# Kernel optimization log

Measured on AMD Instinct MI355X. Metric: run time of the kernel, lower is better.

## Reference

```python
import jax, jax.numpy as jnp
import numpy as np

B, W, H, V, L = 64, 512, 1024, 32000, 2


def setup_inputs() -> dict:
    key = jax.random.key(0)
    ks = jax.random.split(key, 20)
    s = 0.02  # init scale
    n = lambda k, shp: jax.random.normal(k, shp, jnp.float32)
    return {
        "input": jax.random.randint(ks[0], (B, 1), 0, V),
        "h0": n(ks[1], (L, B, H)),
        "c0": n(ks[2], (L, B, H)),
        "encoder_output": n(ks[3], (B, W, H)),
        "embedding": n(ks[4], (V, H)) * s,
        "W_ih0": n(ks[5], (4 * H, H)) * s,
        "W_hh0": n(ks[6], (4 * H, H)) * s,
        "b_ih0": n(ks[7], (4 * H,)) * s,
        "b_hh0": n(ks[8], (4 * H,)) * s,
        "W_ih1": n(ks[9], (4 * H, H)) * s,
        "W_hh1": n(ks[10], (4 * H, H)) * s,
        "b_ih1": n(ks[11], (4 * H,)) * s,
        "b_hh1": n(ks[12], (4 * H,)) * s,
        "att_w": n(ks[13], (2 * H,)) * s,
        "att_b": n(ks[14], (1,)) * s,
        "input_W": n(ks[15], (H, 2 * H)) * s,
        "input_b": n(ks[16], (H,)) * s,
        "out_W": n(ks[17], (V, H)) * s,
        "out_b": n(ks[18], (V,)) * s,
    }


def _lstm_step(x, h, c, W_ih, W_hh, b_ih, b_hh):
    # PyTorch gate order: i, f, g, o
    g = x @ W_ih.T + h @ W_hh.T + b_ih + b_hh
    i, f, gg, o = jnp.split(g, 4, axis=-1)
    c2 = jax.nn.sigmoid(f) * c + jax.nn.sigmoid(i) * jnp.tanh(gg)
    return jax.nn.sigmoid(o) * jnp.tanh(c2), c2


def reference(input, h0, c0, encoder_output, embedding,
              W_ih0, W_hh0, b_ih0, b_hh0, W_ih1, W_hh1, b_ih1, b_hh1,
              att_w, att_b, input_W, input_b, out_W, out_b):
    Hd = h0.shape[-1]
    emb = embedding[input]                       # (B,1,H)
    att_state = h0[-1] * c0[-1]                  # (B,H)
    # Vectorized replacement of the per-word cat+linear loop:
    # att_line(cat(enc_w, att_state)) = enc_w @ w_enc + att_state @ w_st + b
    w_enc, w_st = att_w[:Hd], att_w[Hd:]
    scores = encoder_output @ w_enc + (att_state @ w_st)[:, None] + att_b[0]  # (B,W)
    # Original quirk: weigth starts with a zeros column, then softmax over
    # weigth[:, 0:-1] -> zero column + scores for words 0..W-2 (last dropped).
    zeros = jnp.zeros((scores.shape[0], 1), scores.dtype)
    full = jnp.concatenate([zeros, scores[:, :-1]], axis=1)  # (B,W)
    wts = jax.nn.softmax(full, axis=1)
    ctx = jnp.einsum('bw,bwh->bh', wts, encoder_output)      # (B,H)
    x = jnp.concatenate([ctx, emb[:, 0, :]], axis=-1)        # (B,2H)
    x = x @ input_W.T + input_b                              # (B,H)
    h1, c1 = _lstm_step(x, h0[0], c0[0], W_ih0, W_hh0, b_ih0, b_hh0)
    h2, c2 = _lstm_step(h1, h0[1], c0[1], W_ih1, W_hh1, b_ih1, b_hh1)
    logits = h2 @ out_W.T + out_b                            # (B,V)
    logp = jax.nn.log_softmax(logits, axis=-1)[:, None, :]   # (B,1,V)
    return logp, jnp.stack([h1, h2]), jnp.stack([c1, c2])
```

## Files before the change

### kernel.cpp

```cpp
#include <hip/hip_runtime.h>
#include <hip/hip_bf16.h>

#define Bsz 64
#define Wln 512
#define Hd  1024
#define Vc  32000

typedef short v8s __attribute__((ext_vector_type(8)));
typedef float f32x4 __attribute__((ext_vector_type(4)));

__device__ inline unsigned short f2b(float f) {
  union { float f; unsigned u; } v; v.f = f;
  return (unsigned short)((v.u + 0x8000u) >> 16);
}
__device__ inline float wave_sum(float v) {
  #pragma unroll
  for (int o = 32; o; o >>= 1) v += __shfl_down(v, o);
  return v;
}
__device__ inline float wave_max(float v) {
  #pragma unroll
  for (int o = 32; o; o >>= 1) v = fmaxf(v, __shfl_down(v, o));
  return v;
}
__device__ inline float sigm(float x) { return 1.f / (1.f + expf(-x)); }

__device__ inline v8s cvt_frag(float4 x0, float4 x1) {
  v8s r;
  r[0] = (short)f2b(x0.x); r[1] = (short)f2b(x0.y);
  r[2] = (short)f2b(x0.z); r[3] = (short)f2b(x0.w);
  r[4] = (short)f2b(x1.x); r[5] = (short)f2b(x1.y);
  r[6] = (short)f2b(x1.z); r[7] = (short)f2b(x1.w);
  return r;
}

__global__ __launch_bounds__(256) void k_satt_emb(
    const float* __restrict__ h0, const float* __restrict__ c0,
    const float* __restrict__ att_w, const float* __restrict__ att_b,
    const int* __restrict__ input, const float* __restrict__ emb,
    float* __restrict__ s_att, float* __restrict__ cat)
{
  int b = blockIdx.x, t = threadIdx.x;
  int idx = input[b];
  for (int j = t; j < Hd; j += 256)
    cat[b * 2 * Hd + Hd + j] = emb[(size_t)idx * Hd + j];
  size_t base = (size_t)(Bsz + b) * Hd;
  float s = 0.f;
  for (int j = t; j < Hd; j += 256)
    s += h0[base + j] * c0[base + j] * att_w[Hd + j];
  s = wave_sum(s);
  __shared__ float red[4];
  if ((t & 63) == 0) red[t >> 6] = s;
  __syncthreads();
  if (t == 0) s_att[b] = red[0] + red[1] + red[2] + red[3] + att_b[0];
}

__global__ __launch_bounds__(256) void k_scores(
    const float* __restrict__ enc, const float* __restrict__ att_w,
    const float* __restrict__ s_att, float* __restrict__ scores)
{
  int row = blockIdx.x * 4 + (threadIdx.x >> 6);
  int lane = threadIdx.x & 63;
  const float* p = enc + (size_t)row * Hd + lane * 16;
  const float* w = att_w + lane * 16;
  float s = 0.f;
  #pragma unroll
  for (int c = 0; c < 4; ++c) {
    float4 e = *(const float4*)(p + c * 4);
    float4 ww = *(const float4*)(w + c * 4);
    s += e.x * ww.x + e.y * ww.y + e.z * ww.z + e.w * ww.w;
  }
  s = wave_sum(s);
  if (lane == 0) scores[row] = s + s_att[row >> 9];
}

__global__ __launch_bounds__(512) void k_softmax(
    const float* __restrict__ scores, float* __restrict__ wts)
{
  int b = blockIdx.x, t = threadIdx.x;
  float v = (t == 0) ? 0.f : scores[b * Wln + t - 1];
  __shared__ float redm[8], reds[8];
  float m = wave_max(v);
  if ((t & 63) == 0) redm[t >> 6] = m;
  __syncthreads();
  m = redm[0];
  #pragma unroll
  for (int i = 1; i < 8; ++i) m = fmaxf(m, redm[i]);
  float e = expf(v - m);
  float s = wave_sum(e);
  if ((t & 63) == 0) reds[t >> 6] = s;
  __syncthreads();
  s = reds[0];
  #pragma unroll
  for (int i = 1; i < 8; ++i) s += reds[i];
  wts[b * Wln + t] = e / s;
}

__global__ __launch_bounds__(256) void k_ctx_part(
    const float* __restrict__ wts, const float* __restrict__ enc,
    float* __restrict__ part)
{
  int b = blockIdx.x >> 3, ch = blockIdx.x & 7;
  int t = threadIdx.x;
  __shared__ float w[64];
  if (t < 64) w[t] = wts[b * Wln + ch * 64 + t];
  __syncthreads();
  int h4 = t * 4;
  const float* p = enc + (size_t)b * Wln * Hd + (size_t)ch * 64 * Hd + h4;
  float a0 = 0, a1 = 0, a2 = 0, a3 = 0;
  #pragma unroll 4
  for (int i = 0; i < 64; ++i) {
    float4 e = *(const float4*)(p + (size_t)i * Hd);
    float wi = w[i];
    a0 += wi * e.x; a1 += wi * e.y; a2 += wi * e.z; a3 += wi * e.w;
  }
  float* o = part + ((size_t)b * 8 + ch) * Hd + h4;
  o[0] = a0; o[1] = a1; o[2] = a2; o[3] = a3;
}

__global__ __launch_bounds__(256) void k_ctx_red(
    const float* __restrict__ part, float* __restrict__ cat)
{
  int idx = blockIdx.x * 256 + threadIdx.x;
  int b = idx >> 10, h = idx & 1023;
  float s = 0.f;
  #pragma unroll
  for (int c = 0; c < 8; ++c) s += part[((size_t)b * 8 + c) * Hd + h];
  cat[b * 2 * Hd + h] = s;
}

template<int NS>
__global__ __launch_bounds__(512) void gemm_v4(
    const float* __restrict__ A1, const float* __restrict__ A1b, int sA1,
    const float* __restrict__ B1, int sB1, const float* __restrict__ bias1,
    float* __restrict__ out1,
    const float* __restrict__ A2, const float* __restrict__ A2b, int sA2,
    const float* __restrict__ B2, int sB2, const float* __restrict__ bias2,
    float* __restrict__ out2,
    int N, int nblk1)
{
  constexpr int KS  = 8 / NS;
  constexpr int KSL = 1024 / KS;
  const int tid = threadIdx.x;

  const float *A, *Ab, *B, *bias; float* out; int sA, sB, bid;
  if ((int)blockIdx.x < nblk1) {
    A = A1; Ab = A1b; sA = sA1; B = B1; sB = sB1; bias = bias1; out = out1;
    bid = blockIdx.x;
  } else {
    A = A2; Ab = A2b; sA = sA2; B = B2; sB = sB2; bias = bias2; out = out2;
    bid = blockIdx.x - nblk1;
  }

  __shared__ __align__(16) char pool[131072];

  #pragma unroll
  for (int it = 0; it < 16; ++it) {
    int idx = it * 512 + tid;
    int row = idx >> 7, ch = idx & 127;
    const float* src = A + (size_t)row * sA + ch * 8;
    float4 x0 = *(const float4*)src;
    float4 x1 = *(const float4*)(src + 4);
    if (Ab) {
      const float* s2 = Ab + (size_t)row * sA + ch * 8;
      float4 y0 = *(const float4*)s2;
      float4 y1 = *(const float4*)(s2 + 4);
      x0.x += y0.x; x0.y += y0.y; x0.z += y0.z; x0.w += y0.w;
      x1.x += y1.x; x1.y += y1.y; x1.z += y1.z; x1.w += y1.w;
    }
    *(v8s*)(pool + row * 2048 + ((ch * 16) ^ ((row & 7) << 4))) = cvt_frag(x0, x1);
  }
  __syncthreads();

  const int w = tid >> 6, lane = tid & 63;
  const int r = lane & 15, q = lane >> 4;
  const int nsub = w % NS, kh = w / NS;
  const int n0 = bid * (NS * 16);

  f32x4 acc[4] = {{0,0,0,0},{0,0,0,0},{0,0,0,0},{0,0,0,0}};
  const float* bp = B + (size_t)(n0 + nsub * 16 + r) * sB + kh * KSL + q * 8;
  const int swz = (r & 7) << 4;

  #pragma unroll 4
  for (int kk = 0; kk < KSL / 32; ++kk) {
    float4 b0 = *(const float4*)(bp + kk * 32);
    float4 b1 = *(const float4*)(bp + kk * 32 + 4);
    v8s bf = cvt_frag(b0, b1);
    int cb = ((kh * KSL + kk * 32 + q * 8) * 2) ^ swz;
    #pragma unroll
    for (int m = 0; m < 4; ++m) {
      v8s af = *(const v8s*)(pool + (m * 16 + r) * 2048 + cb);
      acc[m] = __builtin_amdgcn_mfma_f32_16x16x32_bf16(af, bf, acc[m], 0, 0, 0);
    }
  }

  __syncthreads();
  float (*red)[64][17] = (float(*)[64][17])pool;
  #pragma unroll
  for (int m = 0; m < 4; ++m)
    #pragma unroll
    for (int rr = 0; rr < 4; ++rr)
      red[w][lane][m * 4 + rr] = acc[m][rr];
  __syncthreads();

  constexpr int COLS = NS * 16;
  #pragma unroll
  for (int it = 0; it < NS * 2; ++it) {
    int e = it * 512 + tid;
    int cc = e % COLS, rowi = e / COLS;
    int ns2 = cc >> 4, lo = cc & 15;
    int idx = ((rowi >> 4) << 2) + (rowi & 3);
    int le  = (((rowi >> 2) & 3) << 4) + lo;
    float s = 0.f;
    #pragma unroll
    for (int j = 0; j < KS; ++j) s += red[ns2 + j * NS][le][idx];
    float bb = bias ? bias[n0 + cc] : 0.f;
    out[(size_t)rowi * N + n0 + cc] = s + bb;
  }
}

__global__ __launch_bounds__(256) void k_lstm(
    const float* __restrict__ g1, const float* __restrict__ g2,
    const float* __restrict__ c0,
    float* __restrict__ out_h, float* __restrict__ out_c)
{
  int b = blockIdx.x >> 2;
  int j = ((blockIdx.x & 3) << 8) + threadIdx.x;
  const float* ga = g1 + (size_t)b * 4 * Hd;
  const float* gb = g2 + (size_t)b * 4 * Hd;
  float gi = ga[j] + gb[j];
  float gf = ga[Hd + j] + gb[Hd + j];
  float gg = ga[2 * Hd + j] + gb[2 * Hd + j];
  float go = ga[3 * Hd + j] + gb[3 * Hd + j];
  float c = sigm(gf) * c0[(size_t)b * Hd + j] + sigm(gi) * tanhf(gg);
  float h = sigm(go) * tanhf(c);
  out_h[b * Hd + j] = h;
  out_c[b * Hd + j] = c;
}

__global__ __launch_bounds__(1024) void k_logsoftmax(float* __restrict__ lg)
{
  int b = blockIdx.x, t = threadIdx.x;
  float* row = lg + (size_t)b * Vc;
  __shared__ float red[16];
  float m = -1e30f;
  for (int w = t; w < Vc; w += 1024) m = fmaxf(m, row[w]);
  m = wave_max(m);
  if ((t & 63) == 0) red[t >> 6] = m;
  __syncthreads();
  float M = red[0];
  #pragma unroll
  for (int i = 1; i < 16; ++i) M = fmaxf(M, red[i]);
  __syncthreads();
  float s = 0.f;
  for (int w = t; w < Vc; w += 1024) s += expf(row[w] - M);
  s = wave_sum(s);
  if ((t & 63) == 0) red[t >> 6] = s;
  __syncthreads();
  float S = red[0];
  #pragma unroll
  for (int i = 1; i < 16; ++i) S += red[i];
  float lse = M + logf(S);
  for (int w = t; w < Vc; w += 1024) row[w] = row[w] - lse;
}

extern "C" void kernel_launch(void* const* d_in, const int* in_sizes, int n_in,
                              void* d_out, int out_size, void* d_ws, size_t ws_size,
                              hipStream_t stream)
{
  const int*   input = (const int*)d_in[0];
  const float* h0    = (const float*)d_in[1];
  const float* c0    = (const float*)d_in[2];
  const float* enc   = (const float*)d_in[3];
  const float* emb   = (const float*)d_in[4];
  const float* W_ih0 = (const float*)d_in[5];
  const float* W_hh0 = (const float*)d_in[6];
  const float* b_ih0 = (const float*)d_in[7];
  const float* b_hh0 = (const float*)d_in[8];
  const float* W_ih1 = (const float*)d_in[9];
  const float* W_hh1 = (const float*)d_in[10];
  const float* b_ih1 = (const float*)d_in[11];
  const float* b_hh1 = (const float*)d_in[12];
  const float* att_w = (const float*)d_in[13];
  const float* att_b = (const float*)d_in[14];
  const float* inW   = (const float*)d_in[15];
  const float* inb   = (const float*)d_in[16];
  const float* outW  = (const float*)d_in[17];
  const float* outb  = (const float*)d_in[18];
  float* out = (float*)d_out;

  char* sc = (char*)d_out;
  float* g1     = (float*)(sc + 0);
  float* g2     = (float*)(sc + 1048576);
  float* ctxp   = (float*)(sc + 2097152);
  float* cat    = (float*)(sc + 4194304);
  float* x1     = (float*)(sc + 4718592);
  float* x2     = (float*)(sc + 4980736);
  float* scores = (float*)(sc + 5242880);
  float* s_att  = (float*)(sc + 5373952);

  float* out_h = out + (size_t)Bsz * Vc;
  float* out_c = out_h + 2 * Bsz * Hd;
  float* h1 = out_h;
  float* h2 = out_h + Bsz * Hd;

  k_satt_emb<<<Bsz, 256, 0, stream>>>(h0, c0, att_w, att_b, input, emb, s_att, cat);
  k_scores<<<Bsz * Wln / 4, 256, 0, stream>>>(enc, att_w, s_att, scores);
  k_softmax<<<Bsz, 512, 0, stream>>>(scores, scores);
  k_ctx_part<<<Bsz * 8, 256, 0, stream>>>(scores, enc, ctxp);
  k_ctx_red<<<Bsz * Hd / 256, 256, 0, stream>>>(ctxp, cat);

  gemm_v4<1><<<128, 512, 0, stream>>>(
      cat,        nullptr, 2 * Hd, inW,      2 * Hd, inb,     x1,
      cat + Hd,   nullptr, 2 * Hd, inW + Hd, 2 * Hd, nullptr, x2,
      Hd, 64);

  gemm_v4<2><<<256, 512, 0, stream>>>(
      x1, x2,      Hd, W_ih0, Hd, b_ih0, g1,
      h0, nullptr, Hd, W_hh0, Hd, b_hh0, g2,
      4 * Hd, 128);
  k_lstm<<<Bsz * 4, 256, 0, stream>>>(g1, g2, c0, h1, out_c);

  gemm_v4<2><<<256, 512, 0, stream>>>(
      h1,                     nullptr, Hd, W_ih1, Hd, b_ih1, g1,
      h0 + (size_t)Bsz * Hd,  nullptr, Hd, W_hh1, Hd, b_hh1, g2,
      4 * Hd, 128);
  k_lstm<<<Bsz * 4, 256, 0, stream>>>(g1, g2, c0 + (size_t)Bsz * Hd, h2, out_c + Bsz * Hd);

  gemm_v4<4><<<500, 512, 0, stream>>>(
      h2,      nullptr, Hd, outW,    Hd, outb,    out,
      nullptr, nullptr, 0,  nullptr, 0,  nullptr, nullptr,
      Vc, 500);
  k_logsoftmax<<<Bsz, 1024, 0, stream>>>(out);
}
```

Before: 149.8 us.

## Fuse attention kernels and fold context reduction into input GEMM load

Merges the score and state-attention kernels into one launch and folds the softmax into the context-partial kernel, which recomputes the max and sum per chunk block. Adds a mode to the GEMM A-load that sums the 8 context partials, removing the separate reduction kernel and the concat buffer. Log-softmax switches to a single-pass online max/sum, and the GEMM k-loop is fully unrolled. Fewer launches and less global traffic come at the cost of redundant softmax work in every ctx block and heavier GEMM prologue loads.

New measurement: 174.1 us. 16.2% more time.

```diff
diff --git a/kernel.cpp b/kernel.cpp
--- a/kernel.cpp
+++ b/kernel.cpp
@@ -34,122 +34,109 @@
   return r;
 }
 
-__global__ __launch_bounds__(256) void k_satt_emb(
+__global__ __launch_bounds__(256) void k_scores_satt(
+    const float* __restrict__ enc, const float* __restrict__ att_w,
     const float* __restrict__ h0, const float* __restrict__ c0,
-    const float* __restrict__ att_w, const float* __restrict__ att_b,
-    const int* __restrict__ input, const float* __restrict__ emb,
-    float* __restrict__ s_att, float* __restrict__ cat)
-{
-  int b = blockIdx.x, t = threadIdx.x;
-  int idx = input[b];
-  for (int j = t; j < Hd; j += 256)
-    cat[b * 2 * Hd + Hd + j] = emb[(size_t)idx * Hd + j];
-  size_t base = (size_t)(Bsz + b) * Hd;
-  float s = 0.f;
-  for (int j = t; j < Hd; j += 256)
-    s += h0[base + j] * c0[base + j] * att_w[Hd + j];
-  s = wave_sum(s);
+    const float* __restrict__ att_b, const int* __restrict__ input,
+    const float* __restrict__ emb,
+    float* __restrict__ scores, float* __restrict__ s_att,
+    float* __restrict__ embbuf)
+{
   __shared__ float red[4];
-  if ((t & 63) == 0) red[t >> 6] = s;
-  __syncthreads();
-  if (t == 0) s_att[b] = red[0] + red[1] + red[2] + red[3] + att_b[0];
-}
-
-__global__ __launch_bounds__(256) void k_scores(
-    const float* __restrict__ enc, const float* __restrict__ att_w,
-    const float* __restrict__ s_att, float* __restrict__ scores)
-{
-  int row = blockIdx.x * 4 + (threadIdx.x >> 6);
-  int lane = threadIdx.x & 63;
-  const float* p = enc + (size_t)row * Hd + lane * 16;
-  const float* w = att_w + lane * 16;
-  float s = 0.f;
-  #pragma unroll
-  for (int c = 0; c < 4; ++c) {
-    float4 e = *(const float4*)(p + c * 4);
-    float4 ww = *(const float4*)(w + c * 4);
-    s += e.x * ww.x + e.y * ww.y + e.z * ww.z + e.w * ww.w;
-  }
-  s = wave_sum(s);
-  if (lane == 0) scores[row] = s + s_att[row >> 9];
-}
-
-__global__ __launch_bounds__(512) void k_softmax(
-    const float* __restrict__ scores, float* __restrict__ wts)
-{
-  int b = blockIdx.x, t = threadIdx.x;
-  float v = (t == 0) ? 0.f : scores[b * Wln + t - 1];
-  __shared__ float redm[8], reds[8];
-  float m = wave_max(v);
-  if ((t & 63) == 0) redm[t >> 6] = m;
-  __syncthreads();
-  m = redm[0];
-  #pragma unroll
-  for (int i = 1; i < 8; ++i) m = fmaxf(m, redm[i]);
-  float e = expf(v - m);
-  float s = wave_sum(e);
-  if ((t & 63) == 0) reds[t >> 6] = s;
-  __syncthreads();
-  s = reds[0];
-  #pragma unroll
-  for (int i = 1; i < 8; ++i) s += reds[i];
-  wts[b * Wln + t] = e / s;
+  int t = threadIdx.x;
+  if (blockIdx.x < 8192) {
+    int row = blockIdx.x * 4 + (t >> 6);
+    int lane = t & 63;
+    const float* p = enc + (size_t)row * Hd + lane * 16;
+    const float* w = att_w + lane * 16;
+    float s = 0.f;
+    #pragma unroll
+    for (int c = 0; c < 4; ++c) {
+      float4 e = *(const float4*)(p + c * 4);
+      float4 ww = *(const float4*)(w + c * 4);
+      s += e.x * ww.x + e.y * ww.y + e.z * ww.z + e.w * ww.w;
+    }
+    s = wave_sum(s);
+    if (lane == 0) scores[row] = s;
+  } else {
+    int b = blockIdx.x - 8192;
+    int idx = input[b];
+    for (int j = t; j < Hd; j += 256)
+      embbuf[b * Hd + j] = emb[(size_t)idx * Hd + j];
+    size_t base = (size_t)(Bsz + b) * Hd;
+    float s = 0.f;
+    for (int j = t; j < Hd; j += 256)
+      s += h0[base + j] * c0[base + j] * att_w[Hd + j];
+    s = wave_sum(s);
+    if ((t & 63) == 0) red[t >> 6] = s;
+    __syncthreads();
+    if (t == 0) s_att[b] = red[0] + red[1] + red[2] + red[3] + att_b[0];
+  }
 }
 
 __global__ __launch_bounds__(256) void k_ctx_part(
-    const float* __restrict__ wts, const float* __restrict__ enc,
-    float* __restrict__ part)
+    const float* __restrict__ scores, const float* __restrict__ s_att,
+    const float* __restrict__ enc, float* __restrict__ part)
 {
   int b = blockIdx.x >> 3, ch = blockIdx.x & 7;
   int t = threadIdx.x;
+  float sa = s_att[b];
+  const float* sr = scores + b * Wln;
+  int w0 = t * 2, w1 = t * 2 + 1;
+  float v0 = (w0 == 0) ? 0.f : sr[w0 - 1] + sa;
+  float v1 = sr[w1 - 1] + sa;
+  __shared__ float redm[4], reds[4];
+  float m = fmaxf(v0, v1);
+  m = wave_max(m);
+  if ((t & 63) == 0) redm[t >> 6] = m;
+  __syncthreads();
+  float M = fmaxf(fmaxf(redm[0], redm[1]), fmaxf(redm[2], redm[3]));
+  float e = expf(v0 - M) + expf(v1 - M);
+  e = wave_sum(e);
+  if ((t & 63) == 0) reds[t >> 6] = e;
+  __syncthreads();
+  float S = reds[0] + reds[1] + reds[2] + reds[3];
   __shared__ float w[64];
-  if (t < 64) w[t] = wts[b * Wln + ch * 64 + t];
+  if (t < 64) {
+    int wg = ch * 64 + t;
+    float v = (wg == 0) ? 0.f : sr[wg - 1] + sa;
+    w[t] = expf(v - M) / S;
+  }
   __syncthreads();
   int h4 = t * 4;
   const float* p = enc + (size_t)b * Wln * Hd + (size_t)ch * 64 * Hd + h4;
   float a0 = 0, a1 = 0, a2 = 0, a3 = 0;
   #pragma unroll 4
   for (int i = 0; i < 64; ++i) {
-    float4 e = *(const float4*)(p + (size_t)i * Hd);
+    float4 ev = *(const float4*)(p + (size_t)i * Hd);
     float wi = w[i];
-    a0 += wi * e.x; a1 += wi * e.y; a2 += wi * e.z; a3 += wi * e.w;
+    a0 += wi * ev.x; a1 += wi * ev.y; a2 += wi * ev.z; a3 += wi * ev.w;
   }
   float* o = part + ((size_t)b * 8 + ch) * Hd + h4;
   o[0] = a0; o[1] = a1; o[2] = a2; o[3] = a3;
 }
 
-__global__ __launch_bounds__(256) void k_ctx_red(
-    const float* __restrict__ part, float* __restrict__ cat)
-{
-  int idx = blockIdx.x * 256 + threadIdx.x;
-  int b = idx >> 10, h = idx & 1023;
-  float s = 0.f;
-  #pragma unroll
-  for (int c = 0; c < 8; ++c) s += part[((size_t)b * 8 + c) * Hd + h];
-  cat[b * 2 * Hd + h] = s;
-}
-
 template<int NS>
-__global__ __launch_bounds__(512) void gemm_v4(
+__global__ __launch_bounds__(512) void gemm_v5(
     const float* __restrict__ A1, const float* __restrict__ A1b, int sA1,
     const float* __restrict__ B1, int sB1, const float* __restrict__ bias1,
     float* __restrict__ out1,
     const float* __restrict__ A2, const float* __restrict__ A2b, int sA2,
     const float* __restrict__ B2, int sB2, const float* __restrict__ bias2,
     float* __restrict__ out2,
-    int N, int nblk1)
+    int N, int nblk1, int p81)
 {
   constexpr int KS  = 8 / NS;
   constexpr int KSL = 1024 / KS;
   const int tid = threadIdx.x;
 
-  const float *A, *Ab, *B, *bias; float* out; int sA, sB, bid;
+  const float *A, *Ab, *B, *bias; float* out; int sA, sB, bid, p8;
   if ((int)blockIdx.x < nblk1) {
     A = A1; Ab = A1b; sA = sA1; B = B1; sB = sB1; bias = bias1; out = out1;
-    bid = blockIdx.x;
+    bid = blockIdx.x; p8 = p81;
   } else {
     A = A2; Ab = A2b; sA = sA2; B = B2; sB = sB2; bias = bias2; out = out2;
-    bid = blockIdx.x - nblk1;
+    bid = blockIdx.x - nblk1; p8 = 0;
   }
 
   __shared__ __align__(16) char pool[131072];
@@ -158,15 +145,28 @@
   for (int it = 0; it < 16; ++it) {
     int idx = it * 512 + tid;
     int row = idx >> 7, ch = idx & 127;
-    const float* src = A + (size_t)row * sA + ch * 8;
-    float4 x0 = *(const float4*)src;
-    float4 x1 = *(const float4*)(src + 4);
-    if (Ab) {
-      const float* s2 = Ab + (size_t)row * sA + ch * 8;
-      float4 y0 = *(const float4*)s2;
-      float4 y1 = *(const float4*)(s2 + 4);
-      x0.x += y0.x; x0.y += y0.y; x0.z += y0.z; x0.w += y0.w;
-      x1.x += y1.x; x1.y += y1.y; x1.z += y1.z; x1.w += y1.w;
+    float4 x0, x1;
+    if (p8) {
+      const float* src = A + (size_t)row * sA + ch * 8;
+      x0.x = x0.y = x0.z = x0.w = 0.f; x1 = x0;
+      #pragma unroll
+      for (int c = 0; c < 8; ++c) {
+        float4 y0 = *(const float4*)(src + c * Hd);
+        float4 y1 = *(const float4*)(src + c * Hd + 4);
+        x0.x += y0.x; x0.y += y0.y; x0.z += y0.z; x0.w += y0.w;
+        x1.x += y1.x; x1.y += y1.y; x1.z += y1.z; x1.w += y1.w;
+      }
+    } else {
+      const float* src = A + (size_t)row * sA + ch * 8;
+      x0 = *(const float4*)src;
+      x1 = *(const float4*)(src + 4);
+      if (Ab) {
+        const float* s2 = Ab + (size_t)row * sA + ch * 8;
+        float4 y0 = *(const float4*)s2;
+        float4 y1 = *(const float4*)(s2 + 4);
+        x0.x += y0.x; x0.y += y0.y; x0.z += y0.z; x0.w += y0.w;
+        x1.x += y1.x; x1.y += y1.y; x1.z += y1.z; x1.w += y1.w;
+      }
     }
     *(v8s*)(pool + row * 2048 + ((ch * 16) ^ ((row & 7) << 4))) = cvt_frag(x0, x1);
   }
@@ -181,7 +181,7 @@
   const float* bp = B + (size_t)(n0 + nsub * 16 + r) * sB + kh * KSL + q * 8;
   const int swz = (r & 7) << 4;
 
-  #pragma unroll 4
+  #pragma unroll
   for (int kk = 0; kk < KSL / 32; ++kk) {
     float4 b0 = *(const float4*)(bp + kk * 32);
     float4 b1 = *(const float4*)(bp + kk * 32 + 4);
@@ -238,29 +238,38 @@
   out_c[b * Hd + j] = c;
 }
 
+__device__ inline void ms_comb(float& m, float& s, float mo, float so) {
+  if (mo > m) { s = s * expf(m - mo) + so; m = mo; }
+  else        { s += so * expf(mo - m); }
+}
+
 __global__ __launch_bounds__(1024) void k_logsoftmax(float* __restrict__ lg)
 {
   int b = blockIdx.x, t = threadIdx.x;
   float* row = lg + (size_t)b * Vc;
-  __shared__ float red[16];
-  float m = -1e30f;
-  for (int w = t; w < Vc; w += 1024) m = fmaxf(m, row[w]);
-  m = wave_max(m);
-  if ((t & 63) == 0) red[t >> 6] = m;
-  __syncthreads();
-  float M = red[0];
-  #pragma unroll
-  for (int i = 1; i < 16; ++i) M = fmaxf(M, red[i]);
-  __syncthreads();
-  float s = 0.f;
-  for (int w = t; w < Vc; w += 1024) s += expf(row[w] - M);
-  s = wave_sum(s);
-  if ((t & 63) == 0) red[t >> 6] = s;
-  __syncthreads();
-  float S = red[0];
-  #pragma unroll
-  for (int i = 1; i < 16; ++i) S += red[i];
-  float lse = M + logf(S);
+  float m = -1e30f, s = 0.f;
+  for (int w = t; w < Vc; w += 1024) {
+    float v = row[w];
+    if (v > m) { s = s * expf(m - v) + 1.f; m = v; }
+    else       { s += expf(v - m); }
+  }
+  #pragma unroll
+  for (int o = 32; o; o >>= 1) {
+    float mo = __shfl_down(m, o), so = __shfl_down(s, o);
+    ms_comb(m, s, mo, so);
+  }
+  __shared__ float redm[16], reds[16];
+  if ((t & 63) == 0) { redm[t >> 6] = m; reds[t >> 6] = s; }
+  __syncthreads();
+  __shared__ float lse_sh;
+  if (t == 0) {
+    float M = redm[0], S = reds[0];
+    #pragma unroll
+    for (int i = 1; i < 16; ++i) ms_comb(M, S, redm[i], reds[i]);
+    lse_sh = M + logf(S);
+  }
+  __syncthreads();
+  float lse = lse_sh;
   for (int w = t; w < Vc; w += 1024) row[w] = row[w] - lse;
 }
 
@@ -293,43 +302,41 @@
   float* g1     = (float*)(sc + 0);
   float* g2     = (float*)(sc + 1048576);
   float* ctxp   = (float*)(sc + 2097152);
-  float* cat    = (float*)(sc + 4194304);
+  float* embbuf = (float*)(sc + 4194304);
   float* x1     = (float*)(sc + 4718592);
   float* x2     = (float*)(sc + 4980736);
   float* scores = (float*)(sc + 5242880);
-  float* s_att  = (float*)(sc + 5373952);
+  float* s_att  = (float*)(sc + 5505024);
 
   float* out_h = out + (size_t)Bsz * Vc;
   float* out_c = out_h + 2 * Bsz * Hd;
   float* h1 = out_h;
   float* h2 = out_h + Bsz * Hd;
 
-  k_satt_emb<<<Bsz, 256, 0, stream>>>(h0, c0, att_w, att_b, input, emb, s_att, cat);
-  k_scores<<<Bsz * Wln / 4, 256, 0, stream>>>(enc, att_w, s_att, scores);
-  k_softmax<<<Bsz, 512, 0, stream>>>(scores, scores);
-  k_ctx_part<<<Bsz * 8, 256, 0, stream>>>(scores, enc, ctxp);
-  k_ctx_red<<<Bsz * Hd / 256, 256, 0, stream>>>(ctxp, cat);
-
-  gemm_v4<1><<<128, 512, 0, stream>>>(
-      cat,        nullptr, 2 * Hd, inW,      2 * Hd, inb,     x1,
-      cat + Hd,   nullptr, 2 * Hd, inW + Hd, 2 * Hd, nullptr, x2,
-      Hd, 64);
-
-  gemm_v4<2><<<256, 512, 0, stream>>>(
+  k_scores_satt<<<8256, 256, 0, stream>>>(enc, att_w, h0, c0, att_b, input, emb,
+                                          scores, s_att, embbuf);
+  k_ctx_part<<<Bsz * 8, 256, 0, stream>>>(scores, s_att, enc, ctxp);
+
+  gemm_v5<1><<<128, 512, 0, stream>>>(
+      ctxp,   nullptr, 8 * Hd, inW,      2 * Hd, inb,     x1,
+      embbuf, nullptr, Hd,     inW + Hd, 2 * Hd, nullptr, x2,
+      Hd, 64, 1);
+
+  gemm_v5<2><<<256, 512, 0, stream>>>(
       x1, x2,      Hd, W_ih0, Hd, b_ih0, g1,
       h0, nullptr, Hd, W_hh0, Hd, b_hh0, g2,
-      4 * Hd, 128);
+      4 * Hd, 128, 0);
   k_lstm<<<Bsz * 4, 256, 0, stream>>>(g1, g2, c0, h1, out_c);
 
-  gemm_v4<2><<<256, 512, 0, stream>>>(
+  gemm_v5<2><<<256, 512, 0, stream>>>(
       h1,                     nullptr, Hd, W_ih1, Hd, b_ih1, g1,
       h0 + (size_t)Bsz * Hd,  nullptr, Hd, W_hh1, Hd, b_hh1, g2,
-      4 * Hd, 128);
+      4 * Hd, 128, 0);
   k_lstm<<<Bsz * 4, 256, 0, stream>>>(g1, g2, c0 + (size_t)Bsz * Hd, h2, out_c + Bsz * Hd);
 
-  gemm_v4<4><<<500, 512, 0, stream>>>(
+  gemm_v5<4><<<500, 512, 0, stream>>>(
       h2,      nullptr, Hd, outW,    Hd, outb,    out,
       nullptr, nullptr, 0,  nullptr, 0,  nullptr, nullptr,
-      Vc, 500);
+      Vc, 500, 0);
   k_logsoftmax<<<Bsz, 1024, 0, stream>>>(out);
 }
```
